# Performance work log

Measured on AMD Instinct MI355X. Metric: run time of the kernel, lower is better.

Reference implementation:

```python
import jax, jax.numpy as jnp
import numpy as np

EMBED_DIM = 768
NUM_HEADS = 12
HEAD_DIM = EMBED_DIM // NUM_HEADS
SCALE = HEAD_DIM ** -0.5
LN_EPS = 1e-5


def layer_norm(x, gamma, beta):
    mu = jnp.mean(x, axis=-1, keepdims=True)
    var = jnp.var(x, axis=-1, keepdims=True)
    return (x - mu) * jax.lax.rsqrt(var + LN_EPS) * gamma + beta


def setup_inputs() -> dict:
    key = jax.random.key(0)
    ks = jax.random.split(key, 10)
    B, N, M, C = 4, 4096, 256, EMBED_DIM
    inp = {
        "input_tokens": jax.random.normal(ks[0], (B, N, C), dtype=jnp.float32),
        "query_tokens": jax.random.normal(ks[1], (B, M, C), dtype=jnp.float32),
        "Wq": jax.random.normal(ks[2], (C, C), dtype=jnp.float32) * 0.02,
        "bq": jnp.zeros((C,), dtype=jnp.float32),
        "Wk": jax.random.normal(ks[3], (C, C), dtype=jnp.float32) * 0.02,
        "bk": jnp.zeros((C,), dtype=jnp.float32),
        "Wv": jax.random.normal(ks[4], (C, C), dtype=jnp.float32) * 0.02,
        "bv": jnp.zeros((C,), dtype=jnp.float32),
        "gq_ln": jnp.ones((C,), dtype=jnp.float32),
        "bq_ln": jnp.zeros((C,), dtype=jnp.float32),
        "gk_ln": jnp.ones((C,), dtype=jnp.float32),
        "bk_ln": jnp.zeros((C,), dtype=jnp.float32),
    }
    return inp


def reference(input_tokens, query_tokens, Wq, bq, Wk, bk, Wv, bv,
              gq_ln, bq_ln, gk_ln, bk_ln):
    B, N, C = input_tokens.shape
    _, M, _ = query_tokens.shape
    H, D = NUM_HEADS, HEAD_DIM

    # v: Linear only (no LayerNorm on the attn=None path)
    v = (input_tokens @ Wv.T + bv).reshape(B, N, H, D).transpose(0, 2, 1, 3)   # [B,H,N,D]
    # q, k: Linear -> LayerNorm over full embed_dim, then split heads
    q = layer_norm(query_tokens @ Wq.T + bq, gq_ln, bq_ln)
    q = q.reshape(B, M, H, D).transpose(0, 2, 1, 3) * SCALE                    # [B,H,M,D]
    k = layer_norm(input_tokens @ Wk.T + bk, gk_ln, bk_ln)
    k = k.reshape(B, N, H, D).transpose(0, 2, 1, 3)                            # [B,H,N,D]

    attn = jax.nn.softmax(jnp.einsum('bhmd,bhnd->bhmn', q, k), axis=-1)        # [B,H,M,N]
    out = jnp.einsum('bhmn,bhnd->bhmd', attn, v)                               # [B,H,M,D]
    out = out.transpose(0, 2, 1, 3).reshape(B, M, C)
    return (query_tokens + out, attn)
```

## Files before the change

### kernel.cpp

```cpp
#include <hip/hip_runtime.h>
#include <math.h>

#define BB 4
#define NN 4096
#define MM 256
#define CC 768
#define HH 12
#define DD 64
#define SCALEF 0.125f
#define LN_EPSF 1e-5f

typedef __attribute__((ext_vector_type(4))) float f32x4;
typedef __attribute__((ext_vector_type(16))) float f32x16;
typedef __attribute__((ext_vector_type(8))) _Float16 f16x8;
typedef __attribute__((ext_vector_type(4))) _Float16 f16x4;

__device__ __forceinline__ void gldh(const _Float16* g, _Float16* l) {
    __builtin_amdgcn_global_load_lds(
        (const __attribute__((address_space(1))) void*)g,
        (__attribute__((address_space(3))) void*)l, 16, 0, 0);
}

__global__ __launch_bounds__(256) void conv_all(
    const float* __restrict__ x0, _Float16* __restrict__ y0, long long n0,
    const float* __restrict__ x1, _Float16* __restrict__ y1, long long n1,
    const float* __restrict__ x2, _Float16* __restrict__ y2, long long n2,
    const float* __restrict__ x3, _Float16* __restrict__ y3, long long n3,
    const float* __restrict__ x4, _Float16* __restrict__ y4, long long n4)
{
    long long i = ((long long)blockIdx.x * 256 + threadIdx.x) * 8;
    const long long total = n0 + n1 + n2 + n3 + n4;
    const long long stride = (long long)gridDim.x * 256 * 8;
    for (; i < total; i += stride) {
        const float* x; _Float16* y; long long off = i;
        if (off < n0) { x = x0; y = y0; }
        else if ((off -= n0) < n1) { x = x1; y = y1; }
        else if ((off -= n1) < n2) { x = x2; y = y2; }
        else if ((off -= n2) < n3) { x = x3; y = y3; }
        else { off -= n3; x = x4; y = y4; }
        float4 a = *(const float4*)(x + off);
        float4 b = *(const float4*)(x + off + 4);
        f16x8 o;
        o[0] = (_Float16)a.x; o[1] = (_Float16)a.y;
        o[2] = (_Float16)a.z; o[3] = (_Float16)a.w;
        o[4] = (_Float16)b.x; o[5] = (_Float16)b.y;
        o[6] = (_Float16)b.z; o[7] = (_Float16)b.w;
        *(f16x8*)(y + off) = o;
    }
}

__global__ __launch_bounds__(256) void proj_kv_f16(
    const _Float16* __restrict__ Xh,
    const _Float16* __restrict__ X2h,
    const _Float16* __restrict__ Wkh, const _Float16* __restrict__ Wqh,
    const _Float16* __restrict__ Wvh,
    const float* __restrict__ bk, const float* __restrict__ bq,
    const float* __restrict__ bv,
    _Float16* __restrict__ Klin, _Float16* __restrict__ Qlin,
    _Float16* __restrict__ Vth)
{
    __shared__ _Float16 As[2][4096];
    __shared__ _Float16 Bks[2][4096];
    __shared__ _Float16 Bvs[2][4096];

    const int bid = blockIdx.x;
    const _Float16* Ag; const _Float16* Bkg;
    const float* biask; _Float16* outk;
    bool hasV;
    int bm, bn;
    if (bid < 768) {
        bm = bid & 127; bn = bid >> 7;
        Ag = Xh; Bkg = Wkh; biask = bk; outk = Klin; hasV = true;
    } else {
        const int sid = bid - 768;
        bm = sid & 7; bn = sid >> 3;
        Ag = X2h; Bkg = Wqh; biask = bq; outk = Qlin; hasV = false;
    }
    const int row0 = bm * 128, col0 = bn * 128;

    const int tid = threadIdx.x;
    const int w = tid >> 6, lane = tid & 63;
    const int wr = w >> 1, wc = w & 1;
    const int fr = lane & 15, kg = lane >> 4;

    f32x4 acck[4][4], accv[4][4];
#pragma unroll
    for (int m = 0; m < 4; ++m)
#pragma unroll
        for (int n = 0; n < 4; ++n) {
            acck[m][n] = (f32x4){0.f, 0.f, 0.f, 0.f};
            accv[m][n] = (f32x4){0.f, 0.f, 0.f, 0.f};
        }

#define STAGE(sel, kt)                                                           \
    do {                                                                         \
        const int kk = (kt) << 5;                                                \
        _Pragma("unroll")                                                        \
        for (int i = 0; i < 2; ++i) {                                            \
            const int cbase = (i * 4 + w) * 64;                                  \
            const int c = cbase + lane;                                          \
            const int row = c >> 2, ks = (c & 3) << 3;                           \
            gldh(Ag  + (size_t)(row0 + row) * CC + kk + ks, &As[sel][cbase * 8]);\
            gldh(Bkg + (size_t)(col0 + row) * CC + kk + ks, &Bks[sel][cbase * 8]);\
            gldh(Wvh + (size_t)(col0 + row) * CC + kk + ks, &Bvs[sel][cbase * 8]);\
        }                                                                        \
    } while (0)

    STAGE(0, 0);
    int cur = 0;
    const int nk = CC >> 5;
    for (int kt = 0; kt < nk; ++kt) {
        __syncthreads();
        if (kt + 1 < nk) STAGE(cur ^ 1, kt + 1);
        const _Float16* lA = As[cur];
        const _Float16* lBk = Bks[cur];
        const _Float16* lBv = Bvs[cur];
        f16x8 a[4];
#pragma unroll
        for (int m = 0; m < 4; ++m)
            a[m] = *(const f16x8*)(lA + (wr * 64 + m * 16 + fr) * 32 + kg * 8);
#pragma unroll
        for (int n = 0; n < 4; ++n) {
            f16x8 bkf = *(const f16x8*)(lBk + (wc * 64 + n * 16 + fr) * 32 + kg * 8);
            __builtin_amdgcn_s_setprio(1);
#pragma unroll
            for (int m = 0; m < 4; ++m)
                acck[m][n] = __builtin_amdgcn_mfma_f32_16x16x32_f16(
                    a[m], bkf, acck[m][n], 0, 0, 0);
            __builtin_amdgcn_s_setprio(0);
            f16x8 bvf = *(const f16x8*)(lBv + (wc * 64 + n * 16 + fr) * 32 + kg * 8);
            __builtin_amdgcn_s_setprio(1);
#pragma unroll
            for (int m = 0; m < 4; ++m)
                accv[m][n] = __builtin_amdgcn_mfma_f32_16x16x32_f16(
                    a[m], bvf, accv[m][n], 0, 0, 0);
            __builtin_amdgcn_s_setprio(0);
        }
        cur ^= 1;
    }
#undef STAGE

    {
        float bvv[4];
#pragma unroll
        for (int n = 0; n < 4; ++n)
            bvv[n] = biask[col0 + wc * 64 + n * 16 + fr];
#pragma unroll
        for (int m = 0; m < 4; ++m)
#pragma unroll
            for (int n = 0; n < 4; ++n) {
                const int col = col0 + wc * 64 + n * 16 + fr;
#pragma unroll
                for (int r = 0; r < 4; ++r) {
                    const int row = row0 + wr * 64 + m * 16 + kg * 4 + r;
                    outk[(size_t)row * CC + col] = (_Float16)(acck[m][n][r] + bvv[n]);
                }
            }
    }
    if (hasV) {
        const int b = row0 >> 12;
        const int rb = row0 & 4095;
#pragma unroll
        for (int n = 0; n < 4; ++n) {
            const int cg = col0 + wc * 64 + n * 16 + fr;
            const int hh = cg >> 6, d = cg & 63;
            const float bb = bv[cg];
            _Float16* vrow = Vth + ((size_t)((b * HH + hh) * DD + d)) * NN + rb + wr * 64;
#pragma unroll
            for (int m = 0; m < 4; ++m) {
                f16x4 v4;
#pragma unroll
                for (int r = 0; r < 4; ++r)
                    v4[r] = (_Float16)(accv[m][n][r] + bb);
                *(f16x4*)(vrow + m * 16 + kg * 4) = v4;
            }
        }
    }
}

__global__ __launch_bounds__(256) void ln_rows_f16(
    const _Float16* __restrict__ Y, _Float16* __restrict__ outh,
    const float* __restrict__ g, const float* __restrict__ be, const float scale)
{
    const int row = blockIdx.x;
    const _Float16* y = Y + (size_t)row * CC;
    const int tid = threadIdx.x;
    float x0 = (float)y[tid], x1 = (float)y[tid + 256], x2 = (float)y[tid + 512];
    float s = x0 + x1 + x2;
    float q = x0 * x0 + x1 * x1 + x2 * x2;
#pragma unroll
    for (int o = 32; o >= 1; o >>= 1) {
        s += __shfl_xor(s, o, 64);
        q += __shfl_xor(q, o, 64);
    }
    __shared__ float sh_s[4], sh_q[4];
    const int w = tid >> 6;
    if ((tid & 63) == 0) { sh_s[w] = s; sh_q[w] = q; }
    __syncthreads();
    s = sh_s[0] + sh_s[1] + sh_s[2] + sh_s[3];
    q = sh_q[0] + sh_q[1] + sh_q[2] + sh_q[3];
    const float mu  = s * (1.f / 768.f);
    const float var = q * (1.f / 768.f) - mu * mu;
    const float inv = rsqrtf(var + LN_EPSF);
    _Float16* o = outh + (size_t)row * CC;
    o[tid]       = (_Float16)(((x0 - mu) * inv * g[tid]       + be[tid])       * scale);
    o[tid + 256] = (_Float16)(((x1 - mu) * inv * g[tid + 256] + be[tid + 256]) * scale);
    o[tid + 512] = (_Float16)(((x2 - mu) * inv * g[tid + 512] + be[tid + 512]) * scale);
}

__global__ __launch_bounds__(256, 4) void attn_stats(
    const _Float16* __restrict__ Qh,
    const _Float16* __restrict__ Kh,
    float* __restrict__ stats)
{
    __shared__ __align__(16) unsigned char smem[37888];
    _Float16* Kl = (_Float16*)smem;
    _Float16* Ql = (_Float16*)(smem + 32768);
    float (*red)[32][2] = (float(*)[32][2])(smem + 36864);

    const int tid = threadIdx.x;
    const int w = tid >> 6, lane = tid & 63;
    const int l5 = lane >> 5, lm = lane & 31;
    const int bid = blockIdx.x;
    const int mt = bid / 192;
    const int rem = bid % 192;
    const int bh = rem >> 2, ns = rem & 3;
    const int h = bh % HH, b = bh / HH;
    const int qr0 = mt * 32;
    const int nb = ns * 1024;

#define STAGEK(sel, c0)                                                         \
    _Pragma("unroll")                                                           \
    for (int i = 0; i < 4; ++i) {                                               \
        const int L = i * 256 + tid;                                            \
        const int n = L >> 3, pos = L & 7;                                      \
        gldh(Kh + (size_t)(b * NN + (c0) + n) * CC + h * DD + ((pos ^ (n & 7)) << 3), \
             &Kl[(sel) * 8192 + (i * 256 + w * 64) * 8]);                       \
    }

    {
        const int n = tid >> 3, pos = tid & 7;
        gldh(Qh + (size_t)(b * MM + qr0 + n) * CC + h * DD + ((pos ^ (n & 7)) << 3),
             &Ql[(w * 64) * 8]);
    }
    STAGEK(0, nb);
    __syncthreads();
    f16x8 qf[4];
#pragma unroll
    for (int ks = 0; ks < 4; ++ks)
        qf[ks] = *(const f16x8*)&Ql[lm * 64 + (((ks * 2 + l5) ^ (lm & 7)) << 3)];

    const int nl = w * 32 + lm;

    float mrun = -1e30f, srun = 0.f;
    int cur = 0;
    for (int c = 0; c < 8; ++c) {
        if (c) __syncthreads();
        if (c + 1 < 8) STAGEK(cur ^ 1, nb + (c + 1) * 128);
        const _Float16* Kb = Kl + cur * 8192;
        f32x16 s;
#pragma unroll
        for (int r = 0; r < 16; ++r) s[r] = 0.f;
        __builtin_amdgcn_s_setprio(1);
#pragma unroll
        for (int ks = 0; ks < 4; ++ks) {
            f16x8 kf = *(const f16x8*)&Kb[nl * 64 + (((ks * 2 + l5) ^ (nl & 7)) << 3)];
            s = __builtin_amdgcn_mfma_f32_32x32x16_f16(kf, qf[ks], s, 0, 0, 0);
        }
        __builtin_amdgcn_s_setprio(0);
        float cmax = s[0];
#pragma unroll
        for (int r = 1; r < 16; ++r) cmax = fmaxf(cmax, s[r]);
        cmax = fmaxf(cmax, __shfl_xor(cmax, 32, 64));
        const float nm = fmaxf(mrun, cmax);
        float cs = 0.f;
#pragma unroll
        for (int r = 0; r < 16; ++r) cs += __expf(s[r] - nm);
        cs += __shfl_xor(cs, 32, 64);
        srun = srun * __expf(mrun - nm) + cs;
        mrun = nm;
        cur ^= 1;
    }
    if (lane < 32) { red[w][lane][0] = mrun; red[w][lane][1] = srun; }
    __syncthreads();
    if (w == 0 && lane < 32) {
        float M = -1e30f;
#pragma unroll
        for (int ww = 0; ww < 4; ++ww) M = fmaxf(M, red[ww][lane][0]);
        float S = 0.f;
#pragma unroll
        for (int ww = 0; ww < 4; ++ww) S += red[ww][lane][1] * __expf(red[ww][lane][0] - M);
        float* sp = stats + ((size_t)((bh * 8 + mt) * 32 + lane)) * 8 + ns * 2;
        sp[0] = M; sp[1] = S;
    }
#undef STAGEK
}

__global__ __launch_bounds__(256, 2) void attn_main(
    const _Float16* __restrict__ Qh, const _Float16* __restrict__ Kh,
    const _Float16* __restrict__ Vt,
    const float* __restrict__ stats, const float* __restrict__ qtok,
    float* __restrict__ attn, float* __restrict__ out0)
{
    __shared__ __align__(16) unsigned char smem[77824];
    _Float16* Kl = (_Float16*)smem;
    _Float16* Vl = (_Float16*)(smem + 32768);
    _Float16* Ql = (_Float16*)(smem + 65536);
    _Float16* Pl = (_Float16*)(smem + 69632);
    float* rbuf = (float*)smem;

    const int tid = threadIdx.x;
    const int w = tid >> 6, lane = tid & 63;
    const int l5 = lane >> 5, lm = lane & 31;
    const int bh = blockIdx.x % 48;
    const int mt = blockIdx.x / 48;
    const int h = bh % HH, b = bh / HH;
    const int qr0 = mt * 32;

#define STAGEK(sel, c0)                                                         \
    _Pragma("unroll")                                                           \
    for (int i = 0; i < 4; ++i) {                                               \
        const int L = i * 256 + tid;                                            \
        const int n = L >> 3, pos = L & 7;                                      \
        gldh(Kh + (size_t)(b * NN + (c0) + n) * CC + h * DD + ((pos ^ (n & 7)) << 3), \
             &Kl[(sel) * 8192 + (i * 256 + w * 64) * 8]);                       \
    }
#define STAGEV(sel, c0)                                                         \
    _Pragma("unroll")                                                           \
    for (int i = 0; i < 4; ++i) {                                               \
        const int L = i * 256 + tid;                                            \
        const int d = L >> 4, pos = L & 15;                                     \
        const int blk = (pos & 8) | ((pos & 7) ^ (d & 7));                      \
        gldh(Vt + (size_t)(bh * DD + d) * NN + (c0) + blk * 8,                  \
             &Vl[(sel) * 8192 + (i * 256 + w * 64) * 8]);                       \
    }

    float M, invS;
    {
        const float* sp = stats + ((size_t)((bh * 8 + mt) * 32 + lm)) * 8;
        M = -1e30f;
#pragma unroll
        for (int n2 = 0; n2 < 4; ++n2) M = fmaxf(M, sp[n2 * 2]);
        float S = 0.f;
#pragma unroll
        for (int n2 = 0; n2 < 4; ++n2) S += sp[n2 * 2 + 1] * __expf(sp[n2 * 2] - M);
        invS = 1.f / S;
    }

    {
        const int n = tid >> 3, pos = tid & 7;
        gldh(Qh + (size_t)(b * MM + qr0 + n) * CC + h * DD + ((pos ^ (n & 7)) << 3),
             &Ql[(w * 64) * 8]);
    }
    STAGEK(0, 0); STAGEV(0, 0);
    __syncthreads();
    f16x8 qf[4];
#pragma unroll
    for (int ks = 0; ks < 4; ++ks)
        qf[ks] = *(const f16x8*)&Ql[lm * 64 + (((ks * 2 + l5) ^ (lm & 7)) << 3)];

    const int nl = w * 32 + lm;

    f32x16 oacc[2];
#pragma unroll
    for (int dt = 0; dt < 2; ++dt)
#pragma unroll
        for (int r = 0; r < 16; ++r) oacc[dt][r] = 0.f;

    float* attnRow = attn + ((size_t)(bh * MM + qr0 + lm)) * NN;

    int cur = 0;
    for (int c = 0; c < 32; ++c) {
        if (c) {
            asm volatile("s_waitcnt vmcnt(4)" ::: "memory");
            __builtin_amdgcn_s_barrier();
            __builtin_amdgcn_sched_barrier(0);
        }
        if (c + 1 < 32) { STAGEK(cur ^ 1, (c + 1) * 128); STAGEV(cur ^ 1, (c + 1) * 128); }
        __builtin_amdgcn_sched_barrier(0);
        const _Float16* Kb = Kl + cur * 8192;
        const _Float16* Vb = Vl + cur * 8192;
        f32x16 s;
#pragma unroll
        for (int r = 0; r < 16; ++r) s[r] = 0.f;
        __builtin_amdgcn_s_setprio(1);
#pragma unroll
        for (int ks = 0; ks < 4; ++ks) {
            f16x8 kf = *(const f16x8*)&Kb[nl * 64 + (((ks * 2 + l5) ^ (nl & 7)) << 3)];
            s = __builtin_amdgcn_mfma_f32_32x32x16_f16(kf, qf[ks], s, 0, 0, 0);
        }
        __builtin_amdgcn_s_setprio(0);
#pragma unroll
        for (int q = 0; q < 4; ++q) {
            float4 pw;
            f16x4 ph;
#pragma unroll
            for (int r = 0; r < 4; ++r) {
                const float p = __expf(s[q * 4 + r] - M) * invS;
                ((float*)&pw)[r] = p;
                ph[r] = (_Float16)p;
            }
            *(float4*)(attnRow + c * 128 + w * 32 + q * 8 + l5 * 4) = pw;
            const int blk16 = w * 4 + q;
            const int pos = (blk16 & 8) | ((blk16 & 7) ^ (lm & 7));
            *(f16x4*)&Pl[lm * 128 + pos * 8 + l5 * 4] = ph;
        }
        __builtin_amdgcn_s_setprio(1);
#pragma unroll
        for (int ks = 0; ks < 2; ++ks) {
            const int blk16 = w * 4 + ks * 2 + l5;
            const int posP = (blk16 & 8) | ((blk16 & 7) ^ (lm & 7));
            f16x8 pf = *(const f16x8*)&Pl[lm * 128 + posP * 8];
#pragma unroll
            for (int dt = 0; dt < 2; ++dt) {
                const int d = dt * 32 + lm;
                const int posV = (blk16 & 8) | ((blk16 & 7) ^ (d & 7));
                f16x8 vf = *(const f16x8*)&Vb[d * 128 + posV * 8];
                oacc[dt] = __builtin_amdgcn_mfma_f32_32x32x16_f16(pf, vf, oacc[dt], 0, 0, 0);
            }
        }
        __builtin_amdgcn_s_setprio(0);
        cur ^= 1;
    }

    __syncthreads();
#pragma unroll
    for (int dt = 0; dt < 2; ++dt)
#pragma unroll
        for (int r = 0; r < 16; ++r) {
            const int mrow = (r & 3) + 8 * (r >> 2) + 4 * l5;
            rbuf[w * 2048 + mrow * 64 + dt * 32 + lm] = oacc[dt][r];
        }
    __syncthreads();
    {
        const int m = tid >> 3, d0 = (tid & 7) * 8;
        const size_t obase = (size_t)(b * MM + qr0 + m) * CC + h * DD + d0;
#pragma unroll
        for (int j = 0; j < 8; ++j) {
            const int idx = m * 64 + d0 + j;
            float v = rbuf[idx] + rbuf[2048 + idx] + rbuf[4096 + idx] + rbuf[6144 + idx];
            out0[obase + j] = v + qtok[obase + j];
        }
    }
#undef STAGEK
#undef STAGEV
}

extern "C" void kernel_launch(void* const* d_in, const int* in_sizes, int n_in,
                              void* d_out, int out_size, void* d_ws, size_t ws_size,
                              hipStream_t stream) {
    (void)in_sizes; (void)n_in; (void)out_size; (void)ws_size;
    const float* input_tokens = (const float*)d_in[0];
    const float* query_tokens = (const float*)d_in[1];
    const float* Wq   = (const float*)d_in[2];
    const float* bq   = (const float*)d_in[3];
    const float* Wk   = (const float*)d_in[4];
    const float* bk   = (const float*)d_in[5];
    const float* Wv   = (const float*)d_in[6];
    const float* bv   = (const float*)d_in[7];
    const float* gq   = (const float*)d_in[8];
    const float* bqln = (const float*)d_in[9];
    const float* gk   = (const float*)d_in[10];
    const float* bkln = (const float*)d_in[11];

    float* out0 = (float*)d_out;
    float* attn = out0 + (size_t)BB * MM * CC;

    _Float16* hptr = (_Float16*)d_ws;
    _Float16* Klin = hptr;
    _Float16* Qlin = Klin + (size_t)BB * NN * CC;
    _Float16* Xh   = Qlin + (size_t)BB * MM * CC;
    _Float16* X2h  = Xh   + (size_t)BB * NN * CC;
    _Float16* Wkh  = X2h  + (size_t)BB * MM * CC;
    _Float16* Wqh  = Wkh  + (size_t)CC * CC;
    _Float16* Wvh  = Wqh  + (size_t)CC * CC;
    _Float16* Kh   = Wvh  + (size_t)CC * CC;
    _Float16* Qh   = Kh   + (size_t)BB * NN * CC;
    _Float16* Vt   = Qh   + (size_t)BB * MM * CC;
    float* stats   = (float*)(Vt + (size_t)BB * HH * DD * NN);

    conv_all<<<2048, 256, 0, stream>>>(
        input_tokens, Xh, (long long)BB * NN * CC,
        query_tokens, X2h, (long long)BB * MM * CC,
        Wk, Wkh, (long long)CC * CC,
        Wq, Wqh, (long long)CC * CC,
        Wv, Wvh, (long long)CC * CC);

    proj_kv_f16<<<816, 256, 0, stream>>>(Xh, X2h, Wkh, Wqh, Wvh,
                                         bk, bq, bv, Klin, Qlin, Vt);

    ln_rows_f16<<<BB * NN, 256, 0, stream>>>(Klin, Kh, gk, bkln, 1.0f);
    ln_rows_f16<<<BB * MM, 256, 0, stream>>>(Qlin, Qh, gq, bqln, SCALEF);

    attn_stats<<<1536, 256, 0, stream>>>(Qh, Kh, stats);
    attn_main<<<384, 256, 0, stream>>>(Qh, Kh, Vt, stats, query_tokens, attn, out0);
}
```

Baseline: 210.4 us.

## Split attention into two half-batch-head passes for cache locality

The attn_stats and attn_main launches are each split into two launches covering 24 batch-heads apart, and block indexing is reordered so blocks sharing a batch-head run close together. This is meant to keep K/V for the active heads resident in L2/MALL between the stats and main passes. The main loop also replaces the fine-grained vmcnt wait and sched barriers with a plain __syncthreads, which may stall more on outstanding prefetch loads. The extra launches add overhead and halve the grid per launch, so fewer blocks are available to fill the device.

```diff
diff --git a/kernel.cpp b/kernel.cpp
--- a/kernel.cpp
+++ b/kernel.cpp
@@ -211,7 +211,7 @@
 __global__ __launch_bounds__(256, 4) void attn_stats(
     const _Float16* __restrict__ Qh,
     const _Float16* __restrict__ Kh,
-    float* __restrict__ stats)
+    float* __restrict__ stats, const int bh0)
 {
     __shared__ __align__(16) unsigned char smem[37888];
     _Float16* Kl = (_Float16*)smem;
@@ -222,9 +222,9 @@
     const int w = tid >> 6, lane = tid & 63;
     const int l5 = lane >> 5, lm = lane & 31;
     const int bid = blockIdx.x;
-    const int mt = bid / 192;
-    const int rem = bid % 192;
-    const int bh = rem >> 2, ns = rem & 3;
+    const int bh = bh0 + bid % 24;
+    const int t  = bid / 24;
+    const int mt = t >> 2, ns = t & 3;
     const int h = bh % HH, b = bh / HH;
     const int qr0 = mt * 32;
     const int nb = ns * 1024;
@@ -300,7 +300,7 @@
     const _Float16* __restrict__ Qh, const _Float16* __restrict__ Kh,
     const _Float16* __restrict__ Vt,
     const float* __restrict__ stats, const float* __restrict__ qtok,
-    float* __restrict__ attn, float* __restrict__ out0)
+    float* __restrict__ attn, float* __restrict__ out0, const int bh0)
 {
     __shared__ __align__(16) unsigned char smem[77824];
     _Float16* Kl = (_Float16*)smem;
@@ -312,8 +312,8 @@
     const int tid = threadIdx.x;
     const int w = tid >> 6, lane = tid & 63;
     const int l5 = lane >> 5, lm = lane & 31;
-    const int bh = blockIdx.x % 48;
-    const int mt = blockIdx.x / 48;
+    const int bh = bh0 + blockIdx.x % 24;
+    const int mt = blockIdx.x / 24;
     const int h = bh % HH, b = bh / HH;
     const int qr0 = mt * 32;
 
@@ -371,13 +371,8 @@
 
     int cur = 0;
     for (int c = 0; c < 32; ++c) {
-        if (c) {
-            asm volatile("s_waitcnt vmcnt(4)" ::: "memory");
-            __builtin_amdgcn_s_barrier();
-            __builtin_amdgcn_sched_barrier(0);
-        }
+        if (c) __syncthreads();
         if (c + 1 < 32) { STAGEK(cur ^ 1, (c + 1) * 128); STAGEV(cur ^ 1, (c + 1) * 128); }
-        __builtin_amdgcn_sched_barrier(0);
         const _Float16* Kb = Kl + cur * 8192;
         const _Float16* Vb = Vl + cur * 8192;
         f32x16 s;
@@ -392,15 +387,15 @@
         __builtin_amdgcn_s_setprio(0);
 #pragma unroll
         for (int q = 0; q < 4; ++q) {
-            float4 pw;
+            f32x4 pw;
             f16x4 ph;
 #pragma unroll
             for (int r = 0; r < 4; ++r) {
                 const float p = __expf(s[q * 4 + r] - M) * invS;
-                ((float*)&pw)[r] = p;
+                pw[r] = p;
                 ph[r] = (_Float16)p;
             }
-            *(float4*)(attnRow + c * 128 + w * 32 + q * 8 + l5 * 4) = pw;
+            *(f32x4*)(attnRow + c * 128 + w * 32 + q * 8 + l5 * 4) = pw;
             const int blk16 = w * 4 + q;
             const int pos = (blk16 & 8) | ((blk16 & 7) ^ (lm & 7));
             *(f16x4*)&Pl[lm * 128 + pos * 8 + l5 * 4] = ph;
@@ -492,6 +487,8 @@
     ln_rows_f16<<<BB * NN, 256, 0, stream>>>(Klin, Kh, gk, bkln, 1.0f);
     ln_rows_f16<<<BB * MM, 256, 0, stream>>>(Qlin, Qh, gq, bqln, SCALEF);
 
-    attn_stats<<<1536, 256, 0, stream>>>(Qh, Kh, stats);
-    attn_main<<<384, 256, 0, stream>>>(Qh, Kh, Vt, stats, query_tokens, attn, out0);
-}
+    attn_stats<<<768, 256, 0, stream>>>(Qh, Kh, stats, 0);
+    attn_main<<<192, 256, 0, stream>>>(Qh, Kh, Vt, stats, query_tokens, attn, out0, 0);
+    attn_stats<<<768, 256, 0, stream>>>(Qh, Kh, stats, 24);
+    attn_main<<<192, 256, 0, stream>>>(Qh, Kh, Vt, stats, query_tokens, attn, out0, 24);
+}
```

New measurement: 212.9 us. Within noise of the previous version (+1.2%).
